# Performance work log

Measured on AMD Instinct MI355X. Metric: run time of the kernel, lower is better.

Reference implementation:

```python
import jax, jax.numpy as jnp
import numpy as np

C = 256
H = W = 64
B = 8


def setup_inputs() -> dict:
    key = jax.random.key(0)
    ks = jax.random.split(key, 9)
    s = 1.0 / np.sqrt(C)
    x = jax.random.normal(ks[0], (B, C, H, W), dtype=jnp.float32)
    Wq = jax.random.normal(ks[1], (C, C), dtype=jnp.float32) * s
    bq = jnp.zeros((C,), dtype=jnp.float32)
    Wk = jax.random.normal(ks[2], (C, C), dtype=jnp.float32) * s
    bk = jnp.zeros((C,), dtype=jnp.float32)
    Wv = jax.random.normal(ks[3], (C, C), dtype=jnp.float32) * s
    bv = jnp.zeros((C,), dtype=jnp.float32)
    Wp = jax.random.normal(ks[4], (C, C), dtype=jnp.float32) * s
    bp = jnp.zeros((C,), dtype=jnp.float32)
    return {"x": x, "Wq": Wq, "bq": bq, "Wk": Wk, "bk": bk,
            "Wv": Wv, "bv": bv, "Wp": Wp, "bp": bp}


def reference(x, Wq, bq, Wk, bk, Wv, bv, Wp, bp):
    # NOTE: the original forward never calls self.norm, so GroupNorm is omitted.
    Bv_, Cv, Hv, Wv_ = x.shape
    N = Hv * Wv_
    xf = x.reshape(Bv_, Cv, N)  # [B, C, N]
    # 1x1 convs == per-pixel linear over channels
    q = jnp.einsum('oc,bcn->bno', Wq, xf) + bq            # [B, N, C]
    k = jnp.einsum('oc,bcn->bon', Wk, xf) + bk[:, None]   # [B, C, N]
    v = jnp.einsum('oc,bcn->bno', Wv, xf) + bv            # [B, N, C]
    scale = Cv ** (-0.5)
    attn = jnp.einsum('bnc,bcm->bnm', q, k) * scale       # [B, N, N]
    attn = jax.nn.softmax(attn, axis=-1)
    h = jnp.einsum('bnm,bmc->bnc', attn, v)               # [B, N, C]
    h = h.transpose(0, 2, 1).reshape(Bv_, Cv, Hv, Wv_)
    proj = jnp.einsum('oc,bcn->bon', Wp, xf) + bp[:, None]
    proj = proj.reshape(Bv_, Cv, Hv, Wv_)
    # residual uses proj(x) (applied to the INPUT), as in the original code
    return h + proj
```

## Files before the change

### kernel.cpp

```cpp
#include <hip/hip_runtime.h>

typedef __attribute__((ext_vector_type(8))) short short8;
typedef __attribute__((ext_vector_type(4))) short short4v;
typedef __attribute__((ext_vector_type(4))) float floatx4;
typedef unsigned int u32;

#define CC 256
#define NN 4096
#define NB 8

static __device__ __forceinline__ float b2f(ushort u) {
    union { unsigned int i; float f; } c;
    c.i = ((unsigned int)u) << 16;
    return c.f;
}

static __device__ __forceinline__ ushort f2bf(float f) {
    union { float f; unsigned int u; } c;
    c.f = f;
    unsigned int u = c.u;
    u += 0x7fffu + ((u >> 16) & 1u);
    return (ushort)(u >> 16);
}

static __device__ __forceinline__ short8 load8(const void* p, size_t idx, bool isbf) {
    if (isbf) {
        return *(const short8*)((const ushort*)p + idx);
    } else {
        const float* f = (const float*)p + idx;
        floatx4 a = *(const floatx4*)f;
        floatx4 b = *(const floatx4*)(f + 4);
        short8 r;
        #pragma unroll
        for (int j = 0; j < 4; j++) {
            ((ushort*)&r)[j]     = f2bf(a[j]);
            ((ushort*)&r)[j + 4] = f2bf(b[j]);
        }
        return r;
    }
}

static __device__ __forceinline__ float loadS(const void* p, size_t idx, bool isbf) {
    return isbf ? b2f(((const ushort*)p)[idx]) : ((const float*)p)[idx];
}

static __device__ __forceinline__ bool detect_bf16(const void* x) {
    const ushort* xu = (const ushort*)x;
    int cnt = 0;
    #pragma unroll
    for (int j = 0; j < 8; j++) {
        ushort u = xu[(size_t)j * 1048576];
        int e = (u >> 7) & 0xFF;
        cnt += ((e >= 100 && e <= 141) || (u & 0x7FFF) == 0) ? 1 : 0;
    }
    return cnt >= 7;
}

static __device__ __forceinline__ void gll16(const ushort* g, ushort* l) {
    __builtin_amdgcn_global_load_lds(
        (const __attribute__((address_space(1))) u32*)g,
        (__attribute__((address_space(3))) u32*)l, 16, 0, 0);
}

__global__ __launch_bounds__(256) void projkvp(
    const void* __restrict__ x,
    const void* __restrict__ Wk, const void* __restrict__ bk,
    const void* __restrict__ Wv, const void* __restrict__ bv,
    const void* __restrict__ Wp, const void* __restrict__ bp,
    ushort* __restrict__ k_ws, ushort* __restrict__ v_ws,
    float* __restrict__ out, int b0)
{
    __shared__ __align__(16) ushort A_lds[3][64 * 40];
    __shared__ __align__(16) ushort Bt_lds[64 * 40];
    __shared__ __align__(16) ushort T_lds[64 * 72];

    const bool isbf = detect_bf16(x);
    const int tid  = threadIdx.x;
    const int wave = tid >> 6;
    const int lane = tid & 63;
    const int l16  = lane & 15;
    const int quad = lane >> 4;

    const int n0 = blockIdx.x * 64;
    const int o0 = blockIdx.y * 64;
    const int bl = blockIdx.z;
    const int b  = b0 + bl;

    floatx4 zero4 = {0.f, 0.f, 0.f, 0.f};
    floatx4 acc[3][4];
    #pragma unroll
    for (int w = 0; w < 3; w++)
        #pragma unroll
        for (int t = 0; t < 4; t++) acc[w][t] = zero4;

    const void* Ws[3] = {Wk, Wv, Wp};

    for (int k0 = 0; k0 < CC; k0 += 32) {
        __syncthreads();
        {
            int row = tid >> 2, c8 = (tid & 3) * 8;
            #pragma unroll
            for (int w = 0; w < 3; w++)
                *(short8*)&A_lds[w][row * 40 + c8] =
                    load8(Ws[w], (size_t)(o0 + row) * CC + k0 + c8, isbf);
        }
        {
            int c = tid >> 3, n8 = (tid & 7) * 8;
            short8 xv = load8(x, ((size_t)b * CC + k0 + c) * NN + n0 + n8, isbf);
            #pragma unroll
            for (int j = 0; j < 8; j++)
                Bt_lds[(n8 + j) * 40 + c] = ((ushort*)&xv)[j];
        }
        __syncthreads();

        short8 af[3];
        #pragma unroll
        for (int w = 0; w < 3; w++)
            af[w] = *(const short8*)&A_lds[w][(wave * 16 + l16) * 40 + quad * 8];
        #pragma unroll
        for (int t = 0; t < 4; t++) {
            short8 bf = *(const short8*)&Bt_lds[(t * 16 + l16) * 40 + quad * 8];
            #pragma unroll
            for (int w = 0; w < 3; w++)
                acc[w][t] = __builtin_amdgcn_mfma_f32_16x16x32_bf16(af[w], bf, acc[w][t], 0, 0, 0);
        }
    }

    float biasv[3][4];
    const void* Bs[3] = {bk, bv, bp};
    #pragma unroll
    for (int w = 0; w < 3; w++)
        #pragma unroll
        for (int r = 0; r < 4; r++)
            biasv[w][r] = loadS(Bs[w], (size_t)(o0 + wave * 16 + quad * 4 + r), isbf);

    __syncthreads();
    #pragma unroll
    for (int t = 0; t < 4; t++)
        #pragma unroll
        for (int r = 0; r < 4; r++)
            T_lds[(t * 16 + l16) * 72 + wave * 16 + quad * 4 + r] =
                f2bf(acc[0][t][r] + biasv[0][r]);
    __syncthreads();
    for (int u = tid; u < 512; u += 256) {
        int n = u >> 3, o8 = (u & 7) * 8;
        *(short8*)&k_ws[((size_t)bl * NN + n0 + n) * CC + o0 + o8] =
            *(const short8*)&T_lds[n * 72 + o8];
    }

    __syncthreads();
    #pragma unroll
    for (int t = 0; t < 4; t++)
        #pragma unroll
        for (int r = 0; r < 4; r++)
            T_lds[(wave * 16 + quad * 4 + r) * 72 + t * 16 + l16] =
                f2bf(acc[1][t][r] + biasv[1][r]);
    __syncthreads();
    for (int u = tid; u < 512; u += 256) {
        int o = u >> 3, n8 = (u & 7) * 8;
        *(short8*)&v_ws[((size_t)bl * CC + o0 + o) * NN + n0 + n8] =
            *(const short8*)&T_lds[o * 72 + n8];
    }

    #pragma unroll
    for (int t = 0; t < 4; t++)
        #pragma unroll
        for (int r = 0; r < 4; r++)
            out[((size_t)b * CC + o0 + wave * 16 + quad * 4 + r) * NN +
                n0 + t * 16 + l16] = acc[2][t][r] + biasv[2][r];
}

__global__ __launch_bounds__(256) void attn_mfma(
    const void* __restrict__ x,
    const void* __restrict__ Wq, const void* __restrict__ bq,
    const ushort* __restrict__ k_ws, const ushort* __restrict__ v_ws,
    float* __restrict__ out, int b0)
{
    __shared__ __align__(16) ushort lds[18944];
    ushort* K_lds  = lds;
    ushort* Vt_lds = lds + 8192;
    ushort* P_lds  = lds + 16384;
    ushort* Wc_lds = lds;
    ushort* Xt_lds = lds + 10240;
    ushort* Qt_lds = lds;
    float*  Tf     = (float*)lds;

    const bool isbf = detect_bf16(x);
    const int tid  = threadIdx.x;
    const int wave = tid >> 6;
    const int lane = tid & 63;
    const int l16  = lane & 15;
    const int quad = lane >> 4;
    const int bl = blockIdx.y;
    const int b  = b0 + bl;
    const int n0 = blockIdx.x * 64;

    floatx4 zero4 = {0.f, 0.f, 0.f, 0.f};

    {
        floatx4 qacc[16];
        #pragma unroll
        for (int t = 0; t < 16; t++) qacc[t] = zero4;

        for (int k0 = 0; k0 < CC; k0 += 32) {
            __syncthreads();
            #pragma unroll
            for (int i = 0; i < 4; i++) {
                int u = tid + i * 256;
                int row = u >> 2, c8 = (u & 3) * 8;
                *(short8*)&Wc_lds[row * 40 + c8] =
                    load8(Wq, (size_t)row * CC + k0 + c8, isbf);
            }
            {
                int c = tid >> 3, n8 = (tid & 7) * 8;
                short8 xv = load8(x, ((size_t)b * CC + k0 + c) * NN + n0 + n8, isbf);
                #pragma unroll
                for (int j = 0; j < 8; j++)
                    Xt_lds[(n8 + j) * 40 + c] = ((ushort*)&xv)[j];
            }
            __syncthreads();

            short8 af = *(const short8*)&Xt_lds[(wave * 16 + l16) * 40 + quad * 8];
            #pragma unroll
            for (int ct = 0; ct < 16; ct++) {
                short8 bf = *(const short8*)&Wc_lds[(ct * 16 + l16) * 40 + quad * 8];
                qacc[ct] = __builtin_amdgcn_mfma_f32_16x16x32_bf16(af, bf, qacc[ct], 0, 0, 0);
            }
        }

        __syncthreads();
        #pragma unroll
        for (int ct = 0; ct < 16; ct++) {
            float bqv = loadS(bq, (size_t)(ct * 16 + l16), isbf);
            #pragma unroll
            for (int r = 0; r < 4; r++)
                Qt_lds[(wave * 16 + quad * 4 + r) * 264 + ct * 16 + l16] =
                    f2bf((qacc[ct][r] + bqv) * 0.0625f);
        }
    }
    asm volatile("s_waitcnt lgkmcnt(0)" ::: "memory");
    __builtin_amdgcn_sched_barrier(0);
    short8 qf[8];
    #pragma unroll
    for (int s = 0; s < 8; s++)
        qf[s] = *(const short8*)&Qt_lds[(wave * 16 + l16) * 264 + s * 32 + quad * 8];

    const ushort* kp = k_ws + (size_t)bl * NN * CC;
    const ushort* vp = v_ws + (size_t)bl * CC * NN;

    floatx4 Oacc[16];
    #pragma unroll
    for (int t = 0; t < 16; t++) Oacc[t] = zero4;
    float mrow = -1e30f, lrow = 0.f;

    #pragma unroll 1
    for (int it = 0; it < NN / 32; ++it) {
        const int m0 = it * 32;
        __syncthreads();

        #pragma unroll
        for (int i = 0; i < 4; i++) {
            int c = wave * 4 + i;
            {
                int row = c * 2 + (lane >> 5);
                int sw  = (lane & 31) ^ (row & 7);
                gll16(kp + (size_t)(m0 + row) * CC + sw * 8, K_lds + c * 512);
            }
            {
                int ch = c * 16 + (lane >> 2);
                gll16(vp + (size_t)ch * NN + m0 + (lane & 3) * 8, Vt_lds + c * 512);
            }
        }
        __syncthreads();

        floatx4 S[2];
        S[0] = zero4; S[1] = zero4;
        #pragma unroll
        for (int t = 0; t < 2; t++) {
            int row = t * 16 + l16;
            int rsw = row & 7;
            #pragma unroll
            for (int s = 0; s < 8; s++) {
                short8 kf = *(const short8*)&K_lds[row * 256 + ((s * 4 + quad) ^ rsw) * 8];
                S[t] = __builtin_amdgcn_mfma_f32_16x16x32_bf16(kf, qf[s], S[t], 0, 0, 0);
            }
        }

        float mx = fmaxf(fmaxf(fmaxf(S[0][0], S[0][1]), fmaxf(S[0][2], S[0][3])),
                         fmaxf(fmaxf(S[1][0], S[1][1]), fmaxf(S[1][2], S[1][3])));
        mx = fmaxf(mx, __shfl_xor(mx, 16, 64));
        mx = fmaxf(mx, __shfl_xor(mx, 32, 64));

        if (__any(mx - mrow > 8.0f)) {
            float mn = fmaxf(mrow, mx);
            float al = __expf(mrow - mn);
            mrow = mn;
            lrow *= al;
            float a[4];
            #pragma unroll
            for (int r = 0; r < 4; r++) a[r] = __shfl(al, quad * 4 + r, 64);
            #pragma unroll
            for (int ct = 0; ct < 16; ct++)
                #pragma unroll
                for (int r = 0; r < 4; r++)
                    Oacc[ct][r] *= a[r];
        }

        short4v w0, w1;
        float rs = 0.f;
        #pragma unroll
        for (int r = 0; r < 4; r++) {
            float p0 = __expf(S[0][r] - mrow);
            float p1 = __expf(S[1][r] - mrow);
            rs += p0 + p1;
            ((ushort*)&w0)[r] = f2bf(p0);
            ((ushort*)&w1)[r] = f2bf(p1);
        }
        rs += __shfl_xor(rs, 16, 64);
        rs += __shfl_xor(rs, 32, 64);
        lrow += rs;
        {
            int base = wave * 640 + l16 * 40 + quad * 4;
            *(short4v*)&P_lds[base]      = w0;
            *(short4v*)&P_lds[base + 16] = w1;
        }

        asm volatile("s_waitcnt lgkmcnt(0)" ::: "memory");
        __builtin_amdgcn_sched_barrier(0);

        short8 pf = *(const short8*)&P_lds[wave * 640 + l16 * 40 + quad * 8];
        #pragma unroll
        for (int ct = 0; ct < 16; ct++) {
            int ch = ct * 16 + l16;
            short8 vf = *(const short8*)&Vt_lds[ch * 32 + quad * 8];
            Oacc[ct] = __builtin_amdgcn_mfma_f32_16x16x32_bf16(pf, vf, Oacc[ct], 0, 0, 0);
        }
    }

    float li = 1.0f / lrow;
    float linv[4];
    #pragma unroll
    for (int r = 0; r < 4; r++) linv[r] = __shfl(li, quad * 4 + r, 64);

    #pragma unroll
    for (int h = 0; h < 2; h++) {
        __syncthreads();
        #pragma unroll
        for (int ct = h * 8; ct < h * 8 + 8; ct++)
            #pragma unroll
            for (int r = 0; r < 4; r++)
                Tf[(ct * 16 + l16 - h * 128) * 68 + wave * 16 + quad * 4 + r] =
                    Oacc[ct][r] * linv[r];
        __syncthreads();
        #pragma unroll
        for (int i = 0; i < 8; i++) {
            int u = tid + i * 256;
            int row = u >> 4, col4 = (u & 15) * 4;
            size_t gi = ((size_t)b * CC + h * 128 + row) * NN + n0 + col4;
            floatx4 pv = *(const floatx4*)&out[gi];
            floatx4 tv = *(const floatx4*)&Tf[row * 68 + col4];
            pv[0] += tv[0]; pv[1] += tv[1]; pv[2] += tv[2]; pv[3] += tv[3];
            *(floatx4*)&out[gi] = pv;
        }
    }
}

extern "C" void kernel_launch(void* const* d_in, const int* in_sizes, int n_in,
                              void* d_out, int out_size, void* d_ws, size_t ws_size,
                              hipStream_t stream) {
    int xi = 0;
    for (int i = 0; i < n_in; i++)
        if (in_sizes[i] == NB * CC * NN) xi = i;

    const void *x, *Wq, *bq, *Wk, *bk, *Wv, *bv, *Wp, *bp;
    if (xi == 0) {
        x  = d_in[0];
        Wq = d_in[1]; bq = d_in[2];
        Wk = d_in[3]; bk = d_in[4];
        Wv = d_in[5]; bv = d_in[6];
        Wp = d_in[7]; bp = d_in[8];
    } else {
        int wi[4], bi[4], nw = 0, nb = 0;
        for (int i = 0; i < n_in; i++) {
            if (i == xi) continue;
            if (in_sizes[i] == CC * CC) { if (nw < 4) wi[nw++] = i; }
            else                        { if (nb < 4) bi[nb++] = i; }
        }
        x  = d_in[xi];
        Wk = d_in[wi[0]]; Wp = d_in[wi[1]]; Wq = d_in[wi[2]]; Wv = d_in[wi[3]];
        bk = d_in[bi[0]]; bp = d_in[bi[1]]; bq = d_in[bi[2]]; bv = d_in[bi[3]];
    }

    float*  out = (float*)d_out;
    ushort* ws  = (ushort*)d_ws;

    const size_t tsz_b = (size_t)NN * CC;
    int BC = 8;
    while (BC > 1 && (size_t)BC * tsz_b * 2 * 2 > ws_size) BC >>= 1;
    ushort* k_ws = ws;
    ushort* v_ws = ws + (size_t)BC * tsz_b;

    for (int c0 = 0; c0 < NB; c0 += BC) {
        projkvp<<<dim3(NN / 64, CC / 64, BC), dim3(256), 0, stream>>>(
            x, Wk, bk, Wv, bv, Wp, bp, k_ws, v_ws, out, c0);
        attn_mfma<<<dim3(NN / 64, BC), dim3(256), 0, stream>>>(
            x, Wq, bq, k_ws, v_ws, out, c0);
    }
}
```

Baseline: 393.2 us.

## Move Q projection into the projection kernel and load V directly into registers

The Q projection moves out of the attention kernel into the shared K/V/P projection kernel, which now writes a pre-scaled bf16 Q workspace that the attention kernel reads straight into registers. The attention kernel also stops staging V through LDS and instead issues per-lane global loads of V fragments each tile, which shrinks LDS. This removes the redundant per-block Q GEMM prologue and the Wq reloads, at the cost of extra workspace traffic for Q (which may halve the batch chunk size if workspace is tight). It also adds uncoalesced, strided global reads of V in the inner loop.

```diff
diff --git a/kernel.cpp b/kernel.cpp
--- a/kernel.cpp
+++ b/kernel.cpp
@@ -62,15 +62,16 @@
         (__attribute__((address_space(3))) u32*)l, 16, 0, 0);
 }
 
-__global__ __launch_bounds__(256) void projkvp(
+__global__ __launch_bounds__(256) void projkvpq(
     const void* __restrict__ x,
     const void* __restrict__ Wk, const void* __restrict__ bk,
     const void* __restrict__ Wv, const void* __restrict__ bv,
     const void* __restrict__ Wp, const void* __restrict__ bp,
+    const void* __restrict__ Wq, const void* __restrict__ bq,
     ushort* __restrict__ k_ws, ushort* __restrict__ v_ws,
-    float* __restrict__ out, int b0)
+    ushort* __restrict__ q_ws, float* __restrict__ out, int b0)
 {
-    __shared__ __align__(16) ushort A_lds[3][64 * 40];
+    __shared__ __align__(16) ushort A_lds[4][64 * 40];
     __shared__ __align__(16) ushort Bt_lds[64 * 40];
     __shared__ __align__(16) ushort T_lds[64 * 72];
 
@@ -87,20 +88,20 @@
     const int b  = b0 + bl;
 
     floatx4 zero4 = {0.f, 0.f, 0.f, 0.f};
-    floatx4 acc[3][4];
-    #pragma unroll
-    for (int w = 0; w < 3; w++)
+    floatx4 acc[4][4];
+    #pragma unroll
+    for (int w = 0; w < 4; w++)
         #pragma unroll
         for (int t = 0; t < 4; t++) acc[w][t] = zero4;
 
-    const void* Ws[3] = {Wk, Wv, Wp};
+    const void* Ws[4] = {Wk, Wv, Wp, Wq};
 
     for (int k0 = 0; k0 < CC; k0 += 32) {
         __syncthreads();
         {
             int row = tid >> 2, c8 = (tid & 3) * 8;
             #pragma unroll
-            for (int w = 0; w < 3; w++)
+            for (int w = 0; w < 4; w++)
                 *(short8*)&A_lds[w][row * 40 + c8] =
                     load8(Ws[w], (size_t)(o0 + row) * CC + k0 + c8, isbf);
         }
@@ -113,23 +114,23 @@
         }
         __syncthreads();
 
-        short8 af[3];
-        #pragma unroll
-        for (int w = 0; w < 3; w++)
+        short8 af[4];
+        #pragma unroll
+        for (int w = 0; w < 4; w++)
             af[w] = *(const short8*)&A_lds[w][(wave * 16 + l16) * 40 + quad * 8];
         #pragma unroll
         for (int t = 0; t < 4; t++) {
             short8 bf = *(const short8*)&Bt_lds[(t * 16 + l16) * 40 + quad * 8];
             #pragma unroll
-            for (int w = 0; w < 3; w++)
+            for (int w = 0; w < 4; w++)
                 acc[w][t] = __builtin_amdgcn_mfma_f32_16x16x32_bf16(af[w], bf, acc[w][t], 0, 0, 0);
         }
     }
 
-    float biasv[3][4];
-    const void* Bs[3] = {bk, bv, bp};
-    #pragma unroll
-    for (int w = 0; w < 3; w++)
+    float biasv[4][4];
+    const void* Bs[4] = {bk, bv, bp, bq};
+    #pragma unroll
+    for (int w = 0; w < 4; w++)
         #pragma unroll
         for (int r = 0; r < 4; r++)
             biasv[w][r] = loadS(Bs[w], (size_t)(o0 + wave * 16 + quad * 4 + r), isbf);
@@ -153,6 +154,20 @@
     for (int t = 0; t < 4; t++)
         #pragma unroll
         for (int r = 0; r < 4; r++)
+            T_lds[(t * 16 + l16) * 72 + wave * 16 + quad * 4 + r] =
+                f2bf((acc[3][t][r] + biasv[3][r]) * 0.0625f);
+    __syncthreads();
+    for (int u = tid; u < 512; u += 256) {
+        int n = u >> 3, o8 = (u & 7) * 8;
+        *(short8*)&q_ws[((size_t)bl * NN + n0 + n) * CC + o0 + o8] =
+            *(const short8*)&T_lds[n * 72 + o8];
+    }
+
+    __syncthreads();
+    #pragma unroll
+    for (int t = 0; t < 4; t++)
+        #pragma unroll
+        for (int r = 0; r < 4; r++)
             T_lds[(wave * 16 + quad * 4 + r) * 72 + t * 16 + l16] =
                 f2bf(acc[1][t][r] + biasv[1][r]);
     __syncthreads();
@@ -171,21 +186,14 @@
 }
 
 __global__ __launch_bounds__(256) void attn_mfma(
-    const void* __restrict__ x,
-    const void* __restrict__ Wq, const void* __restrict__ bq,
-    const ushort* __restrict__ k_ws, const ushort* __restrict__ v_ws,
-    float* __restrict__ out, int b0)
+    const ushort* __restrict__ q_ws, const ushort* __restrict__ k_ws,
+    const ushort* __restrict__ v_ws, float* __restrict__ out, int b0)
 {
-    __shared__ __align__(16) ushort lds[18944];
-    ushort* K_lds  = lds;
-    ushort* Vt_lds = lds + 8192;
-    ushort* P_lds  = lds + 16384;
-    ushort* Wc_lds = lds;
-    ushort* Xt_lds = lds + 10240;
-    ushort* Qt_lds = lds;
-    float*  Tf     = (float*)lds;
-
-    const bool isbf = detect_bf16(x);
+    __shared__ __align__(16) ushort lds[17408];
+    ushort* K_lds = lds;
+    ushort* P_lds = lds + 8192;
+    float*  Tf    = (float*)lds;
+
     const int tid  = threadIdx.x;
     const int wave = tid >> 6;
     const int lane = tid & 63;
@@ -197,53 +205,11 @@
 
     floatx4 zero4 = {0.f, 0.f, 0.f, 0.f};
 
-    {
-        floatx4 qacc[16];
-        #pragma unroll
-        for (int t = 0; t < 16; t++) qacc[t] = zero4;
-
-        for (int k0 = 0; k0 < CC; k0 += 32) {
-            __syncthreads();
-            #pragma unroll
-            for (int i = 0; i < 4; i++) {
-                int u = tid + i * 256;
-                int row = u >> 2, c8 = (u & 3) * 8;
-                *(short8*)&Wc_lds[row * 40 + c8] =
-                    load8(Wq, (size_t)row * CC + k0 + c8, isbf);
-            }
-            {
-                int c = tid >> 3, n8 = (tid & 7) * 8;
-                short8 xv = load8(x, ((size_t)b * CC + k0 + c) * NN + n0 + n8, isbf);
-                #pragma unroll
-                for (int j = 0; j < 8; j++)
-                    Xt_lds[(n8 + j) * 40 + c] = ((ushort*)&xv)[j];
-            }
-            __syncthreads();
-
-            short8 af = *(const short8*)&Xt_lds[(wave * 16 + l16) * 40 + quad * 8];
-            #pragma unroll
-            for (int ct = 0; ct < 16; ct++) {
-                short8 bf = *(const short8*)&Wc_lds[(ct * 16 + l16) * 40 + quad * 8];
-                qacc[ct] = __builtin_amdgcn_mfma_f32_16x16x32_bf16(af, bf, qacc[ct], 0, 0, 0);
-            }
-        }
-
-        __syncthreads();
-        #pragma unroll
-        for (int ct = 0; ct < 16; ct++) {
-            float bqv = loadS(bq, (size_t)(ct * 16 + l16), isbf);
-            #pragma unroll
-            for (int r = 0; r < 4; r++)
-                Qt_lds[(wave * 16 + quad * 4 + r) * 264 + ct * 16 + l16] =
-                    f2bf((qacc[ct][r] + bqv) * 0.0625f);
-        }
-    }
-    asm volatile("s_waitcnt lgkmcnt(0)" ::: "memory");
-    __builtin_amdgcn_sched_barrier(0);
+    const ushort* qp = q_ws + ((size_t)bl * NN + n0 + wave * 16 + l16) * CC;
     short8 qf[8];
     #pragma unroll
     for (int s = 0; s < 8; s++)
-        qf[s] = *(const short8*)&Qt_lds[(wave * 16 + l16) * 264 + s * 32 + quad * 8];
+        qf[s] = *(const short8*)&qp[s * 32 + quad * 8];
 
     const ushort* kp = k_ws + (size_t)bl * NN * CC;
     const ushort* vp = v_ws + (size_t)bl * CC * NN;
@@ -261,15 +227,9 @@
         #pragma unroll
         for (int i = 0; i < 4; i++) {
             int c = wave * 4 + i;
-            {
-                int row = c * 2 + (lane >> 5);
-                int sw  = (lane & 31) ^ (row & 7);
-                gll16(kp + (size_t)(m0 + row) * CC + sw * 8, K_lds + c * 512);
-            }
-            {
-                int ch = c * 16 + (lane >> 2);
-                gll16(vp + (size_t)ch * NN + m0 + (lane & 3) * 8, Vt_lds + c * 512);
-            }
+            int row = c * 2 + (lane >> 5);
+            int sw  = (lane & 31) ^ (row & 7);
+            gll16(kp + (size_t)(m0 + row) * CC + sw * 8, K_lds + c * 512);
         }
         __syncthreads();
 
@@ -285,6 +245,11 @@
                 S[t] = __builtin_amdgcn_mfma_f32_16x16x32_bf16(kf, qf[s], S[t], 0, 0, 0);
             }
         }
+
+        short8 vreg[16];
+        #pragma unroll
+        for (int ct = 0; ct < 16; ct++)
+            vreg[ct] = *(const short8*)&vp[(size_t)(ct * 16 + l16) * NN + m0 + quad * 8];
 
         float mx = fmaxf(fmaxf(fmaxf(S[0][0], S[0][1]), fmaxf(S[0][2], S[0][3])),
                          fmaxf(fmaxf(S[1][0], S[1][1]), fmaxf(S[1][2], S[1][3])));
@@ -330,11 +295,8 @@
 
         short8 pf = *(const short8*)&P_lds[wave * 640 + l16 * 40 + quad * 8];
         #pragma unroll
-        for (int ct = 0; ct < 16; ct++) {
-            int ch = ct * 16 + l16;
-            short8 vf = *(const short8*)&Vt_lds[ch * 32 + quad * 8];
-            Oacc[ct] = __builtin_amdgcn_mfma_f32_16x16x32_bf16(pf, vf, Oacc[ct], 0, 0, 0);
-        }
+        for (int ct = 0; ct < 16; ct++)
+            Oacc[ct] = __builtin_amdgcn_mfma_f32_16x16x32_bf16(pf, vreg[ct], Oacc[ct], 0, 0, 0);
     }
 
     float li = 1.0f / lrow;
@@ -396,14 +358,15 @@
 
     const size_t tsz_b = (size_t)NN * CC;
     int BC = 8;
-    while (BC > 1 && (size_t)BC * tsz_b * 2 * 2 > ws_size) BC >>= 1;
+    while (BC > 1 && (size_t)BC * tsz_b * 2 * 3 > ws_size) BC >>= 1;
     ushort* k_ws = ws;
     ushort* v_ws = ws + (size_t)BC * tsz_b;
+    ushort* q_ws = ws + 2 * (size_t)BC * tsz_b;
 
     for (int c0 = 0; c0 < NB; c0 += BC) {
-        projkvp<<<dim3(NN / 64, CC / 64, BC), dim3(256), 0, stream>>>(
-            x, Wk, bk, Wv, bv, Wp, bp, k_ws, v_ws, out, c0);
+        projkvpq<<<dim3(NN / 64, CC / 64, BC), dim3(256), 0, stream>>>(
+            x, Wk, bk, Wv, bv, Wp, bp, Wq, bq, k_ws, v_ws, q_ws, out, c0);
         attn_mfma<<<dim3(NN / 64, BC), dim3(256), 0, stream>>>(
-            x, Wq, bq, k_ws, v_ws, out, c0);
-    }
-}
+            q_ws, k_ws, v_ws, out, c0);
+    }
+}
```

After: 695.3 us. 76.8% more time.
